# Optimization experiments

Measured on AMD Instinct MI355X. Metric: run time of the kernel, lower is better.

## Reference

```python
import jax, jax.numpy as jnp
import numpy as np
from jax import lax

RATIO = 2.0
ITERATIONS = 1


def setup_inputs() -> dict:
    key = jax.random.key(0)
    k1, k2 = jax.random.split(key)
    N, H, W = 64, 512, 512
    x = jax.random.normal(k1, (N, H, W), dtype=jnp.float32)  # logits
    y = jax.random.randint(k2, (N, H, W), 0, 2, dtype=jnp.int32)  # binary labels
    return {"x": x, "y": y}


def _erode(m):
    # cv2.erode with 3x3 all-ones kernel == 3x3 min-pool; cv2 default border
    # value for erode is +inf, matching reduce_window's init_value padding.
    return lax.reduce_window(m, jnp.inf, lax.min, (1, 3, 3), (1, 1, 1), 'SAME')


def _dilate(m):
    # cv2.dilate == 3x3 max-pool; default border value -inf == init_value pad.
    return lax.reduce_window(m, -jnp.inf, lax.max, (1, 3, 3), (1, 1, 1), 'SAME')


def reference(x, y):
    yf = y.astype(x.dtype)
    # elementwise BCE-with-logits (reduction='none'), numerically stable
    loss = jnp.maximum(x, 0.0) - x * yf + jnp.log1p(jnp.exp(-jnp.abs(x)))
    m = (y > 0).astype(x.dtype)  # [N,H,W] binary mask
    ero, dil = m, m
    for _ in range(ITERATIONS):
        ero = _erode(ero)
        dil = _dilate(dil)
    border = dil - ero  # 1 on border pixels, 0 elsewhere
    w = border * RATIO + (1.0 - border)
    return (loss * w).mean()
```

## Files before the change

kernel.cpp:

```cpp
#include <hip/hip_runtime.h>
#include <math.h>

#define NIMG 64
#define HH 512
#define WW 512
#define TR 16
#define LR (TR + 2)
#define LSTRIDE 130
#define NBLOCKS (NIMG * (HH / TR))
#define INV_TOTAL (1.0f / 16777216.0f)

typedef unsigned int u32;
typedef unsigned long long u64;

__device__ __forceinline__ u32 flags4(int4 yv) {
    u32 f = (yv.x > 0) ? 1u : 2u;
    f |= ((yv.y > 0) ? 1u : 2u) << 8;
    f |= ((yv.z > 0) ? 1u : 2u) << 16;
    f |= ((yv.w > 0) ? 1u : 2u) << 24;
    return f;
}

__global__ __launch_bounds__(256, 8) void border_loss_main(
    const float* __restrict__ x, const int* __restrict__ y,
    float* __restrict__ part, int atomic_mode)
{
    __shared__ __align__(16) u32 flags[LR][LSTRIDE];
    __shared__ float wsum[4];

    const int tid  = threadIdx.x;
    const int lane = tid & 63;
    const int wv   = tid >> 6;
    const int b    = blockIdx.x;
    const int n    = b >> 5;
    const int R0   = (b & 31) * TR;
    const int base = n * (HH * WW);
    const int*   __restrict__ yb = y + base;
    const float* __restrict__ xb = x + base;

    if (tid < 2 * LR) {
        flags[tid >> 1][(tid & 1) ? (LSTRIDE - 1) : 0] = 0u;
    }

    for (int it = 0; it < 9; ++it) {
        const int idx = tid + (it << 8);
        const int j   = idx >> 7;
        const int g   = idx & 127;
        const int gr  = R0 - 1 + j;
        u32 f = 0u;
        if ((unsigned)gr < (unsigned)HH) {
            const int4 yv = *(const int4*)(yb + gr * WW + (g << 2));
            f = flags4(yv);
        }
        flags[j][g + 1] = f;
    }
    __syncthreads();

    float acc = 0.0f;
    for (int it = 0; it < 4; ++it) {
        const int idx = tid + (it << 8);
        const int r   = idx >> 6;
        const int c   = idx & 63;
        const int jt  = r;
        const int d   = c << 1;

        const u64 t0 = *(const u64*)&flags[jt    ][d];
        const u64 t1 = *(const u64*)&flags[jt    ][d + 2];
        const u64 c0 = *(const u64*)&flags[jt + 1][d];
        const u64 c1 = *(const u64*)&flags[jt + 1][d + 2];
        const u64 b0 = *(const u64*)&flags[jt + 2][d];
        const u64 b1 = *(const u64*)&flags[jt + 2][d + 2];

        const float* xr = xb + (R0 + r) * WW + (c << 3);
        const float4 xa = *(const float4*)(xr);
        const float4 xd = *(const float4*)(xr + 4);

        const u64 A = t0 | c0 | b0;
        const u64 B = t1 | c1 | b1;
        const u64 cen = (A >> 32) | (B << 32);
        const u64 lb  = (A >> 24) & 0xffull;
        const u64 rb  = ((B >> 32) & 0xffull) << 56;
        const u64 h   = cen | (cen << 8) | (cen >> 8) | lb | rb;
        const u64 border = h & (h >> 1) & 0x0101010101010101ull;
        const u64 m64    = (c0 >> 32) | (c1 << 32);

        {
            const float xf = xa.x;
            const float lg = __logf(1.0f + __expf(-fabsf(xf)));
            const float ls = fmaxf(xf, 0.0f) - ((m64 & 1ull) ? xf : 0.0f) + lg;
            acc = fmaf(ls, (border & 1ull) ? 2.0f : 1.0f, acc);
        }
        {
            const float xf = xa.y;
            const float lg = __logf(1.0f + __expf(-fabsf(xf)));
            const float ls = fmaxf(xf, 0.0f) - ((m64 >> 8 & 1ull) ? xf : 0.0f) + lg;
            acc = fmaf(ls, (border >> 8 & 1ull) ? 2.0f : 1.0f, acc);
        }
        {
            const float xf = xa.z;
            const float lg = __logf(1.0f + __expf(-fabsf(xf)));
            const float ls = fmaxf(xf, 0.0f) - ((m64 >> 16 & 1ull) ? xf : 0.0f) + lg;
            acc = fmaf(ls, (border >> 16 & 1ull) ? 2.0f : 1.0f, acc);
        }
        {
            const float xf = xa.w;
            const float lg = __logf(1.0f + __expf(-fabsf(xf)));
            const float ls = fmaxf(xf, 0.0f) - ((m64 >> 24 & 1ull) ? xf : 0.0f) + lg;
            acc = fmaf(ls, (border >> 24 & 1ull) ? 2.0f : 1.0f, acc);
        }
        {
            const float xf = xd.x;
            const float lg = __logf(1.0f + __expf(-fabsf(xf)));
            const float ls = fmaxf(xf, 0.0f) - ((m64 >> 32 & 1ull) ? xf : 0.0f) + lg;
            acc = fmaf(ls, (border >> 32 & 1ull) ? 2.0f : 1.0f, acc);
        }
        {
            const float xf = xd.y;
            const float lg = __logf(1.0f + __expf(-fabsf(xf)));
            const float ls = fmaxf(xf, 0.0f) - ((m64 >> 40 & 1ull) ? xf : 0.0f) + lg;
            acc = fmaf(ls, (border >> 40 & 1ull) ? 2.0f : 1.0f, acc);
        }
        {
            const float xf = xd.z;
            const float lg = __logf(1.0f + __expf(-fabsf(xf)));
            const float ls = fmaxf(xf, 0.0f) - ((m64 >> 48 & 1ull) ? xf : 0.0f) + lg;
            acc = fmaf(ls, (border >> 48 & 1ull) ? 2.0f : 1.0f, acc);
        }
        {
            const float xf = xd.w;
            const float lg = __logf(1.0f + __expf(-fabsf(xf)));
            const float ls = fmaxf(xf, 0.0f) - ((m64 >> 56 & 1ull) ? xf : 0.0f) + lg;
            acc = fmaf(ls, (border >> 56 & 1ull) ? 2.0f : 1.0f, acc);
        }
    }

    #pragma unroll
    for (int off = 32; off > 0; off >>= 1)
        acc += __shfl_down(acc, off);
    __syncthreads();
    if (lane == 0) wsum[wv] = acc;
    __syncthreads();
    if (tid == 0) {
        const float t = wsum[0] + wsum[1] + wsum[2] + wsum[3];
        if (atomic_mode) atomicAdd(part, t * INV_TOTAL);
        else             part[blockIdx.x] = t;
    }
}

__global__ __launch_bounds__(256) void border_loss_reduce(
    const float* __restrict__ part, float* __restrict__ out)
{
    __shared__ float wsum[4];
    float t = 0.0f;
    for (int i = threadIdx.x; i < NBLOCKS; i += 256) t += part[i];
    #pragma unroll
    for (int off = 32; off > 0; off >>= 1)
        t += __shfl_down(t, off);
    if ((threadIdx.x & 63) == 0) wsum[threadIdx.x >> 6] = t;
    __syncthreads();
    if (threadIdx.x == 0)
        out[0] = (wsum[0] + wsum[1] + wsum[2] + wsum[3]) * INV_TOTAL;
}

__global__ void border_loss_zero(float* out) { out[0] = 0.0f; }

extern "C" void kernel_launch(void* const* d_in, const int* in_sizes, int n_in,
                              void* d_out, int out_size, void* d_ws, size_t ws_size,
                              hipStream_t stream)
{
    const float* x = (const float*)d_in[0];
    const int*   y = (const int*)d_in[1];
    float* out = (float*)d_out;

    if (ws_size >= (size_t)NBLOCKS * sizeof(float)) {
        float* part = (float*)d_ws;
        border_loss_main<<<NBLOCKS, 256, 0, stream>>>(x, y, part, 0);
        border_loss_reduce<<<1, 256, 0, stream>>>(part, out);
    } else {
        border_loss_zero<<<1, 1, 0, stream>>>(out);
        border_loss_main<<<NBLOCKS, 256, 0, stream>>>(x, y, out, 1);
    }
}
```

Measured before the change: 146.6 us.

## Replace LDS halo tile with per-wave register sliding window and shuffles

Each wavefront now processes an 8-row strip spanning a full 512-wide image row, holding three rows of packed label flags in registers. Horizontal neighbours come from lane shuffles and vertical neighbours from rotating registers, which removes the shared-memory flag tile and its block barrier. The next row's x and y are prefetched while the current row is computed. The trade-off is a higher vertical halo re-read ratio (10 label rows per 8 output rows) and lower occupancy bounds.

After: 200.7 us. 36.9% more time.

```diff
diff --git a/kernel.cpp b/kernel.cpp
--- a/kernel.cpp
+++ b/kernel.cpp
@@ -4,140 +4,129 @@
 #define NIMG 64
 #define HH 512
 #define WW 512
-#define TR 16
-#define LR (TR + 2)
-#define LSTRIDE 130
-#define NBLOCKS (NIMG * (HH / TR))
+#define TR 8
+#define SPI (HH / TR)
+#define NSTRIP (NIMG * SPI)
+#define WPB 4
+#define NBLK (NSTRIP / WPB)
 #define INV_TOTAL (1.0f / 16777216.0f)
 
 typedef unsigned int u32;
 typedef unsigned long long u64;
 
-__device__ __forceinline__ u32 flags4(int4 yv) {
-    u32 f = (yv.x > 0) ? 1u : 2u;
-    f |= ((yv.y > 0) ? 1u : 2u) << 8;
-    f |= ((yv.z > 0) ? 1u : 2u) << 16;
-    f |= ((yv.w > 0) ? 1u : 2u) << 24;
-    return f;
+__device__ __forceinline__ u64 pack8(const int4 a, const int4 b) {
+    u32 lo = ((a.x > 0) ? 1u : 2u)
+           | (((a.y > 0) ? 1u : 2u) << 8)
+           | (((a.z > 0) ? 1u : 2u) << 16)
+           | (((a.w > 0) ? 1u : 2u) << 24);
+    u32 hi = ((b.x > 0) ? 1u : 2u)
+           | (((b.y > 0) ? 1u : 2u) << 8)
+           | (((b.z > 0) ? 1u : 2u) << 16)
+           | (((b.w > 0) ? 1u : 2u) << 24);
+    return (u64)lo | ((u64)hi << 32);
 }
 
-__global__ __launch_bounds__(256, 8) void border_loss_main(
+__device__ __forceinline__ u64 hor3(u64 f, int lane) {
+    const u32 hi = (u32)(f >> 32);
+    const u32 lo = (u32)f;
+    const u32 lw = __shfl_up(hi, 1);
+    const u32 rw = __shfl_down(lo, 1);
+    const u64 left  = (lane == 0)  ? 0ull : (u64)(lw >> 24);
+    const u64 right = (lane == 63) ? 0ull : ((u64)(rw & 0xffu) << 56);
+    return f | (f << 8) | (f >> 8) | left | right;
+}
+
+__global__ __launch_bounds__(256, 4) void border_loss_main(
     const float* __restrict__ x, const int* __restrict__ y,
     float* __restrict__ part, int atomic_mode)
 {
-    __shared__ __align__(16) u32 flags[LR][LSTRIDE];
-    __shared__ float wsum[4];
+    __shared__ float wsum[WPB];
 
     const int tid  = threadIdx.x;
     const int lane = tid & 63;
     const int wv   = tid >> 6;
-    const int b    = blockIdx.x;
-    const int n    = b >> 5;
-    const int R0   = (b & 31) * TR;
+    const int s    = blockIdx.x * WPB + wv;
+    const int n    = s >> 6;
+    const int R0   = (s & (SPI - 1)) * TR;
     const int base = n * (HH * WW);
-    const int*   __restrict__ yb = y + base;
-    const float* __restrict__ xb = x + base;
+    const int*   __restrict__ yp = y + base + (lane << 3);
+    const float* __restrict__ xp = x + base + (lane << 3);
 
-    if (tid < 2 * LR) {
-        flags[tid >> 1][(tid & 1) ? (LSTRIDE - 1) : 0] = 0u;
+    u64 f_a;
+    if (R0 > 0) {
+        const int4* p = (const int4*)(yp + (R0 - 1) * WW);
+        f_a = pack8(p[0], p[1]);
+    } else {
+        f_a = 0ull;
+    }
+    u64 h_a = hor3(f_a, lane);
+
+    u64 f_b;
+    {
+        const int4* p = (const int4*)(yp + R0 * WW);
+        f_b = pack8(p[0], p[1]);
+    }
+    u64 h_b = hor3(f_b, lane);
+
+    int4 yc0, yc1;
+    bool vc = true;
+    {
+        const int4* p = (const int4*)(yp + (R0 + 1) * WW);
+        yc0 = p[0]; yc1 = p[1];
+    }
+    float4 xc0, xc1;
+    {
+        const float4* p = (const float4*)(xp + R0 * WW);
+        xc0 = p[0]; xc1 = p[1];
     }
 
-    for (int it = 0; it < 9; ++it) {
-        const int idx = tid + (it << 8);
-        const int j   = idx >> 7;
-        const int g   = idx & 127;
-        const int gr  = R0 - 1 + j;
-        u32 f = 0u;
-        if ((unsigned)gr < (unsigned)HH) {
-            const int4 yv = *(const int4*)(yb + gr * WW + (g << 2));
-            f = flags4(yv);
+    float acc = 0.0f;
+    #pragma unroll
+    for (int r = 0; r < TR; ++r) {
+        int4 yn0, yn1; bool vn = false;
+        float4 xn0, xn1;
+        if (r < TR - 1) {
+            const int g = R0 + r + 2;
+            vn = (g < HH);
+            if (vn) {
+                const int4* p = (const int4*)(yp + g * WW);
+                yn0 = p[0]; yn1 = p[1];
+            } else {
+                yn0 = make_int4(0, 0, 0, 0); yn1 = make_int4(0, 0, 0, 0);
+            }
+            const float4* p = (const float4*)(xp + (R0 + r + 1) * WW);
+            xn0 = p[0]; xn1 = p[1];
+        } else {
+            yn0 = make_int4(0, 0, 0, 0); yn1 = make_int4(0, 0, 0, 0);
+            xn0 = make_float4(0.f, 0.f, 0.f, 0.f);
+            xn1 = make_float4(0.f, 0.f, 0.f, 0.f);
         }
-        flags[j][g + 1] = f;
-    }
-    __syncthreads();
 
-    float acc = 0.0f;
-    for (int it = 0; it < 4; ++it) {
-        const int idx = tid + (it << 8);
-        const int r   = idx >> 6;
-        const int c   = idx & 63;
-        const int jt  = r;
-        const int d   = c << 1;
+        const u64 f_c = vc ? pack8(yc0, yc1) : 0ull;
+        const u64 h_c = hor3(f_c, lane);
 
-        const u64 t0 = *(const u64*)&flags[jt    ][d];
-        const u64 t1 = *(const u64*)&flags[jt    ][d + 2];
-        const u64 c0 = *(const u64*)&flags[jt + 1][d];
-        const u64 c1 = *(const u64*)&flags[jt + 1][d + 2];
-        const u64 b0 = *(const u64*)&flags[jt + 2][d];
-        const u64 b1 = *(const u64*)&flags[jt + 2][d + 2];
+        const u64 v      = h_a | h_b | h_c;
+        const u64 border = v & (v >> 1) & 0x0101010101010101ull;
+        const u64 m64    = f_b;
 
-        const float* xr = xb + (R0 + r) * WW + (c << 3);
-        const float4 xa = *(const float4*)(xr);
-        const float4 xd = *(const float4*)(xr + 4);
+        #define PX(XF, K) { \
+            const float xf = (XF); \
+            const float lg = __logf(1.0f + __expf(-fabsf(xf))); \
+            const float ls = fmaxf(xf, 0.0f) \
+                           - (((m64 >> (K)) & 1ull) ? xf : 0.0f) + lg; \
+            acc = fmaf(ls, ((border >> (K)) & 1ull) ? 2.0f : 1.0f, acc); }
+        PX(xc0.x,  0) PX(xc0.y,  8) PX(xc0.z, 16) PX(xc0.w, 24)
+        PX(xc1.x, 32) PX(xc1.y, 40) PX(xc1.z, 48) PX(xc1.w, 56)
+        #undef PX
 
-        const u64 A = t0 | c0 | b0;
-        const u64 B = t1 | c1 | b1;
-        const u64 cen = (A >> 32) | (B << 32);
-        const u64 lb  = (A >> 24) & 0xffull;
-        const u64 rb  = ((B >> 32) & 0xffull) << 56;
-        const u64 h   = cen | (cen << 8) | (cen >> 8) | lb | rb;
-        const u64 border = h & (h >> 1) & 0x0101010101010101ull;
-        const u64 m64    = (c0 >> 32) | (c1 << 32);
-
-        {
-            const float xf = xa.x;
-            const float lg = __logf(1.0f + __expf(-fabsf(xf)));
-            const float ls = fmaxf(xf, 0.0f) - ((m64 & 1ull) ? xf : 0.0f) + lg;
-            acc = fmaf(ls, (border & 1ull) ? 2.0f : 1.0f, acc);
-        }
-        {
-            const float xf = xa.y;
-            const float lg = __logf(1.0f + __expf(-fabsf(xf)));
-            const float ls = fmaxf(xf, 0.0f) - ((m64 >> 8 & 1ull) ? xf : 0.0f) + lg;
-            acc = fmaf(ls, (border >> 8 & 1ull) ? 2.0f : 1.0f, acc);
-        }
-        {
-            const float xf = xa.z;
-            const float lg = __logf(1.0f + __expf(-fabsf(xf)));
-            const float ls = fmaxf(xf, 0.0f) - ((m64 >> 16 & 1ull) ? xf : 0.0f) + lg;
-            acc = fmaf(ls, (border >> 16 & 1ull) ? 2.0f : 1.0f, acc);
-        }
-        {
-            const float xf = xa.w;
-            const float lg = __logf(1.0f + __expf(-fabsf(xf)));
-            const float ls = fmaxf(xf, 0.0f) - ((m64 >> 24 & 1ull) ? xf : 0.0f) + lg;
-            acc = fmaf(ls, (border >> 24 & 1ull) ? 2.0f : 1.0f, acc);
-        }
-        {
-            const float xf = xd.x;
-            const float lg = __logf(1.0f + __expf(-fabsf(xf)));
-            const float ls = fmaxf(xf, 0.0f) - ((m64 >> 32 & 1ull) ? xf : 0.0f) + lg;
-            acc = fmaf(ls, (border >> 32 & 1ull) ? 2.0f : 1.0f, acc);
-        }
-        {
-            const float xf = xd.y;
-            const float lg = __logf(1.0f + __expf(-fabsf(xf)));
-            const float ls = fmaxf(xf, 0.0f) - ((m64 >> 40 & 1ull) ? xf : 0.0f) + lg;
-            acc = fmaf(ls, (border >> 40 & 1ull) ? 2.0f : 1.0f, acc);
-        }
-        {
-            const float xf = xd.z;
-            const float lg = __logf(1.0f + __expf(-fabsf(xf)));
-            const float ls = fmaxf(xf, 0.0f) - ((m64 >> 48 & 1ull) ? xf : 0.0f) + lg;
-            acc = fmaf(ls, (border >> 48 & 1ull) ? 2.0f : 1.0f, acc);
-        }
-        {
-            const float xf = xd.w;
-            const float lg = __logf(1.0f + __expf(-fabsf(xf)));
-            const float ls = fmaxf(xf, 0.0f) - ((m64 >> 56 & 1ull) ? xf : 0.0f) + lg;
-            acc = fmaf(ls, (border >> 56 & 1ull) ? 2.0f : 1.0f, acc);
-        }
+        h_a = h_b; h_b = h_c; f_b = f_c;
+        yc0 = yn0; yc1 = yn1; vc = vn;
+        xc0 = xn0; xc1 = xn1;
     }
 
     #pragma unroll
     for (int off = 32; off > 0; off >>= 1)
         acc += __shfl_down(acc, off);
-    __syncthreads();
     if (lane == 0) wsum[wv] = acc;
     __syncthreads();
     if (tid == 0) {
@@ -152,7 +141,7 @@
 {
     __shared__ float wsum[4];
     float t = 0.0f;
-    for (int i = threadIdx.x; i < NBLOCKS; i += 256) t += part[i];
+    for (int i = threadIdx.x; i < NBLK; i += 256) t += part[i];
     #pragma unroll
     for (int off = 32; off > 0; off >>= 1)
         t += __shfl_down(t, off);
@@ -172,12 +161,12 @@
     const int*   y = (const int*)d_in[1];
     float* out = (float*)d_out;
 
-    if (ws_size >= (size_t)NBLOCKS * sizeof(float)) {
+    if (ws_size >= (size_t)NBLK * sizeof(float)) {
         float* part = (float*)d_ws;
-        border_loss_main<<<NBLOCKS, 256, 0, stream>>>(x, y, part, 0);
+        border_loss_main<<<NBLK, 256, 0, stream>>>(x, y, part, 0);
         border_loss_reduce<<<1, 256, 0, stream>>>(part, out);
     } else {
         border_loss_zero<<<1, 1, 0, stream>>>(out);
-        border_loss_main<<<NBLOCKS, 256, 0, stream>>>(x, y, out, 1);
+        border_loss_main<<<NBLK, 256, 0, stream>>>(x, y, out, 1);
     }
 }
```
